# Optimization experiments

Measured on AMD Instinct MI355X. Metric: run time of the kernel, lower is better.

The kernel has to match this reference:

```python
import jax, jax.numpy as jnp
import numpy as np

B, T, C = 2, 2048, 2048
H = 16
D = C // H  # head_dim = 128


def rotate_half(x):
    x1, x2 = jnp.split(x, 2, axis=-1)
    return jnp.concatenate([-x2, x1], axis=-1)


def apply_rotary(q, k, cos, sin):
    # q,k: (B,H,T,D); cos,sin: (T,D/2)
    cos2 = jnp.concatenate([cos, cos], axis=-1)[None, None]  # (1,1,T,D)
    sin2 = jnp.concatenate([sin, sin], axis=-1)[None, None]
    return q * cos2 + rotate_half(q) * sin2, k * cos2 + rotate_half(k) * sin2


def setup_inputs() -> dict:
    key = jax.random.key(0)
    k1, k2, k3, k4 = jax.random.split(key, 4)
    x = jax.random.normal(k1, (B, T, C), dtype=jnp.float32)
    w_qkv = jax.random.normal(k2, (C, 3 * C), dtype=jnp.float32) * (C ** -0.5)
    w_out = jax.random.normal(k3, (C, C), dtype=jnp.float32) * (C ** -0.5)
    pos = jnp.arange(T, dtype=jnp.float32)[:, None]
    inv_freq = 1.0 / (10000.0 ** (jnp.arange(0, D, 2, dtype=jnp.float32) / D))  # (D/2,)
    ang = pos * inv_freq[None, :]  # (T, D/2)
    return {"x": x, "w_qkv": w_qkv, "w_out": w_out,
            "cos": jnp.cos(ang), "sin": jnp.sin(ang)}


def reference(x, w_qkv, w_out, cos, sin):
    b, t, c = x.shape
    qkv = x @ w_qkv  # (B,T,3C)
    qkv = qkv.reshape(b, t, 3, H, D)
    q, k, v = qkv[:, :, 0], qkv[:, :, 1], qkv[:, :, 2]  # (B,T,H,D)
    q = q.transpose(0, 2, 1, 3)  # (B,H,T,D)
    k = k.transpose(0, 2, 1, 3)
    v = v.transpose(0, 2, 1, 3)
    q, k = apply_rotary(q, k, cos, sin)
    scale = 1.0 / jnp.sqrt(jnp.asarray(D, dtype=x.dtype))
    scores = jnp.einsum('bhqd,bhkd->bhqk', q, k) * scale  # (B,H,T,T)
    causal = jnp.tril(jnp.ones((t, t), dtype=bool))
    scores = jnp.where(causal[None, None], scores, jnp.asarray(-jnp.inf, dtype=scores.dtype))
    attn = jax.nn.softmax(scores, axis=-1)
    out = jnp.einsum('bhqk,bhkd->bhqd', attn, v)  # (B,H,T,D)
    out = out.transpose(0, 2, 1, 3).reshape(b, t, c)
    return out @ w_out
```

## Files before the change

### kernel.cpp

```cpp
#include <hip/hip_runtime.h>


typedef __attribute__((ext_vector_type(8))) short short8;
typedef __attribute__((ext_vector_type(4))) float floatx4;
typedef __attribute__((ext_vector_type(4))) unsigned int uint4v;

#define MFMA16(a, b, c) __builtin_amdgcn_mfma_f32_16x16x32_bf16(a, b, c, 0, 0, 0)

__device__ inline unsigned short f2bf(float f) {
    union { float f; unsigned int i; } v; v.f = f;
    unsigned int r = v.i + 0x7fff + ((v.i >> 16) & 1);
    return (unsigned short)(r >> 16);
}

__device__ inline void gl2lds16(const unsigned short* g, unsigned short* l) {
    __builtin_amdgcn_global_load_lds(
        (const __attribute__((address_space(1))) unsigned int*)g,
        (__attribute__((address_space(3))) unsigned int*)l, 16, 0, 0);
}

__device__ __forceinline__ void bar_lds_only() {
    asm volatile("s_waitcnt lgkmcnt(0)" ::: "memory");
    __builtin_amdgcn_sched_barrier(0);
    __builtin_amdgcn_s_barrier();
    __builtin_amdgcn_sched_barrier(0);
}

__global__ __launch_bounds__(256) void cvt_k(const float* __restrict__ in,
                                             unsigned short* __restrict__ out, int n) {
    int i = (blockIdx.x * 256 + threadIdx.x) * 8;
    if (i + 7 < n) {
        float4 v0 = *(const float4*)(&in[i]);
        float4 v1 = *(const float4*)(&in[i + 4]);
        ushort4 o0, o1;
        o0.x = f2bf(v0.x); o0.y = f2bf(v0.y); o0.z = f2bf(v0.z); o0.w = f2bf(v0.w);
        o1.x = f2bf(v1.x); o1.y = f2bf(v1.y); o1.z = f2bf(v1.z); o1.w = f2bf(v1.w);
        *(ushort4*)(&out[i])     = o0;
        *(ushort4*)(&out[i + 4]) = o1;
    } else {
        for (int j = i; j < n; j++) out[j] = f2bf(in[j]);
    }
}

__global__ __launch_bounds__(256) void transpose_f2b_k(const float* __restrict__ in,
                                                       unsigned short* __restrict__ out,
                                                       int R, int Cc) {
    __shared__ unsigned short tile[32][33];
    int ct = blockIdx.x * 32;
    int rt = blockIdx.y * 32;
    int tx = threadIdx.x & 31;
    int ty = threadIdx.x >> 5;
#pragma unroll
    for (int i = 0; i < 32; i += 8)
        tile[ty + i][tx] = f2bf(in[(size_t)(rt + ty + i) * Cc + ct + tx]);
    __syncthreads();
#pragma unroll
    for (int i = 0; i < 32; i += 8)
        out[(size_t)(ct + ty + i) * R + rt + tx] = tile[tx][ty + i];
}

__global__ __launch_bounds__(256) void transpose_v_k(const unsigned short* __restrict__ qkv,
                                                     unsigned short* __restrict__ VT) {
    __shared__ unsigned short tile[32][33];
    int t0 = blockIdx.x * 32;
    int d0 = blockIdx.y * 32;
    int bh = blockIdx.z;
    int b = bh >> 4, h = bh & 15;
    int tx = threadIdx.x & 31;
    int ty = threadIdx.x >> 5;
#pragma unroll
    for (int i = 0; i < 32; i += 8)
        tile[ty + i][tx] =
            qkv[((size_t)(b * 2048 + t0 + ty + i) * 3 + 2) * 2048 + h * 128 + d0 + tx];
    __syncthreads();
#pragma unroll
    for (int i = 0; i < 32; i += 8)
        VT[((size_t)bh * 128 + d0 + ty + i) * 2048 + t0 + tx] = tile[tx][ty + i];
}

__global__ __launch_bounds__(256) void rotary_k(unsigned short* qkv,
                                                const float* __restrict__ cosT,
                                                const float* __restrict__ sinT) {
    int idx = blockIdx.x * 256 + threadIdx.x;
    int d    = idx & 63;
    int h    = (idx >> 6) & 15;
    int part = (idx >> 10) & 1;
    int t    = (idx >> 11) & 2047;
    int b    = idx >> 22;
    size_t base = ((size_t)(b * 2048 + t) * 3 + part) * 2048 + h * 128;
    float c = cosT[t * 64 + d];
    float s = sinT[t * 64 + d];
    union { unsigned int i; float f; } u1, u2;
    u1.i = ((unsigned int)qkv[base + d]) << 16;
    u2.i = ((unsigned int)qkv[base + d + 64]) << 16;
    float x1 = u1.f, x2 = u2.f;
    qkv[base + d]      = f2bf(x1 * c - x2 * s);
    qkv[base + d + 64] = f2bf(x2 * c + x1 * s);
}

template <bool OUTF32>
__global__ __launch_bounds__(256) void gemm_bt(const unsigned short* __restrict__ A, long lda,
                                               const unsigned short* __restrict__ Bt,
                                               void* __restrict__ Co, long ldc,
                                               int M, int N, int K) {
    __shared__ unsigned short a_lds[2][128 * 32];
    __shared__ unsigned short b_lds[2][128 * 32];
    int m0 = blockIdx.y * 128, n0 = blockIdx.x * 128;
    int tid = threadIdx.x;
    int lane = tid & 63, w = tid >> 6;
    int wm = (w >> 1) * 64, wn = (w & 1) * 64;
    int lr = lane & 15, quad = lane >> 4, lk = quad * 8;

    floatx4 acc[4][4];
    floatx4 zero4 = {0.f, 0.f, 0.f, 0.f};
#pragma unroll
    for (int i = 0; i < 4; i++)
#pragma unroll
        for (int j = 0; j < 4; j++) acc[i][j] = zero4;

    auto stage = [&](int k0, int buf) {
#pragma unroll
        for (int i = 0; i < 2; i++) {
            int c = w * 128 + i * 64 + lane;
            int row = c >> 2, seg = (c & 3) * 8;
            gl2lds16(&A[(size_t)(m0 + row) * lda + k0 + seg], &a_lds[buf][c * 8]);
            gl2lds16(&Bt[(size_t)(n0 + row) * K + k0 + seg], &b_lds[buf][c * 8]);
        }
    };

    int nt = K >> 5;
    stage(0, 0);
    __syncthreads();
    for (int t = 0; t < nt; t++) {
        int buf = t & 1;
        if (t + 1 < nt) stage((t + 1) * 32, buf ^ 1);
        short8 af[4], bfr[4];
#pragma unroll
        for (int i = 0; i < 4; i++)
            af[i] = *(const short8*)(&a_lds[buf][(wm + i * 16 + lr) * 32 + lk]);
#pragma unroll
        for (int j = 0; j < 4; j++)
            bfr[j] = *(const short8*)(&b_lds[buf][(wn + j * 16 + lr) * 32 + lk]);
#pragma unroll
        for (int i = 0; i < 4; i++)
#pragma unroll
            for (int j = 0; j < 4; j++)
                acc[i][j] = MFMA16(af[i], bfr[j], acc[i][j]);
        __syncthreads();
    }
#pragma unroll
    for (int i = 0; i < 4; i++)
#pragma unroll
        for (int j = 0; j < 4; j++)
#pragma unroll
            for (int r = 0; r < 4; r++) {
                int row = m0 + wm + i * 16 + quad * 4 + r;
                int col = n0 + wn + j * 16 + lr;
                if (OUTF32)
                    ((float*)Co)[(size_t)row * ldc + col] = acc[i][j][r];
                else
                    ((unsigned short*)Co)[(size_t)row * ldc + col] = f2bf(acc[i][j][r]);
            }
}

__device__ __forceinline__ void attn_core(const short8 (&qf)[4], floatx4 (&o_acc)[8],
                                          floatx4& o_l,
                                          float (&m_i)[4],
                                          const unsigned short* kb_lds,
                                          const unsigned short* vb_lds,
                                          unsigned short* p_w,
                                          int qrow0, int tk0, int lr, int quad, int lk) {
    floatx4 zero4 = {0.f, 0.f, 0.f, 0.f};
    const float scale = 0.08838834764831845f;

    floatx4 s[4];
#pragma unroll
    for (int n = 0; n < 4; n++) {
        s[n] = zero4;
#pragma unroll
        for (int c = 0; c < 4; c++) {
            short8 kb = *(const short8*)(
                &kb_lds[(n * 16 + lr) * 128 + (((c * 4 + quad) ^ lr) * 8)]);
            s[n] = MFMA16(qf[c], kb, s[n]);
        }
    }

    float rmax[4];
#pragma unroll
    for (int r = 0; r < 4; r++) {
        int tqr = qrow0 + quad * 4 + r;
        float mx = -1e30f;
#pragma unroll
        for (int n = 0; n < 4; n++) {
            int tk = tk0 + n * 16 + lr;
            float sv = s[n][r] * scale;
            sv = (tk > tqr) ? -1e30f : sv;
            s[n][r] = sv;
            mx = fmaxf(mx, sv);
        }
        rmax[r] = mx;
    }
#pragma unroll
    for (int off = 1; off < 16; off <<= 1)
#pragma unroll
        for (int r = 0; r < 4; r++)
            rmax[r] = fmaxf(rmax[r], __shfl_xor(rmax[r], off, 64));

    float alpha[4];
#pragma unroll
    for (int r = 0; r < 4; r++) {
        float mn = fmaxf(m_i[r], rmax[r]);
        alpha[r] = __expf(m_i[r] - mn);
        m_i[r] = mn;
    }
#pragma unroll
    for (int n = 0; n < 4; n++)
#pragma unroll
        for (int r = 0; r < 4; r++) {
            float p = __expf(s[n][r] - m_i[r]);
            p_w[(quad * 4 + r) * 72 + n * 16 + lr] = f2bf(p);
        }

#pragma unroll
    for (int dt = 0; dt < 8; dt++)
#pragma unroll
        for (int r = 0; r < 4; r++) o_acc[dt][r] *= alpha[r];
#pragma unroll
    for (int r = 0; r < 4; r++) o_l[r] *= alpha[r];

    short8 pa[2];
#pragma unroll
    for (int kc = 0; kc < 2; kc++)
        pa[kc] = *(const short8*)(&p_w[lr * 72 + kc * 32 + lk]);
#pragma unroll
    for (int dt = 0; dt < 8; dt++) {
#pragma unroll
        for (int kc = 0; kc < 2; kc++) {
            short8 vb = *(const short8*)(
                &vb_lds[(dt * 16 + lr) * 64 + (((kc * 4 + quad) ^ (lr & 7)) * 8)]);
            o_acc[dt] = MFMA16(pa[kc], vb, o_acc[dt]);
        }
    }
#pragma unroll
    for (int kc = 0; kc < 2; kc++) {
        short8 vb1 = *(const short8*)(&vb_lds[128 * 64 + (kc * 4 + quad) * 8]);
        o_l = MFMA16(pa[kc], vb1, o_l);
    }
}

__global__ __launch_bounds__(512, 4) void attn_fast(unsigned short* qkv,
                                                    const unsigned short* __restrict__ VT) {
    const int T = 2048, Cc = 2048, Dd = 128;
    int xx = blockIdx.x;
    int qt = (xx & 1) ? (xx >> 1) : (15 - (xx >> 1));
    int bh = blockIdx.y;
    int b = bh >> 4, h = bh & 15;
    int tid = threadIdx.x, lane = tid & 63, w = tid >> 6;
    int lr = lane & 15, quad = lane >> 4, lk = quad * 8;
    int t0 = qt * 128;

    __shared__ __align__(16) unsigned short k_lds[64 * 128];
    __shared__ __align__(16) unsigned short v_lds[129 * 64];
    __shared__ __align__(16) unsigned short p_lds[8][16][72];

    if (tid < 64) v_lds[128 * 64 + tid] = 0x3F80;

    short8 qf[4];
    {
        size_t qrow = (size_t)(b * T + t0 + w * 16 + lr) * 3 * Cc + h * Dd;
#pragma unroll
        for (int c = 0; c < 4; c++)
            qf[c] = *(const short8*)(&qkv[qrow + c * 32 + lk]);
    }

    floatx4 o_acc[8];
    floatx4 zero4 = {0.f, 0.f, 0.f, 0.f};
#pragma unroll
    for (int i = 0; i < 8; i++) o_acc[i] = zero4;
    floatx4 o_l = zero4;
    float m_i[4];
#pragma unroll
    for (int r = 0; r < 4; r++) m_i[r] = -1e30f;

    int krow[2], kslot[2], vrow[2], vslot[2];
#pragma unroll
    for (int i = 0; i < 2; i++) {
        int c = i * 512 + tid;
        krow[i] = c >> 4; kslot[i] = c & 15;
        vrow[i] = c >> 3; vslot[i] = c & 7;
    }
    uint4v kA[2], vA[2];
    auto gload = [&](int kt) {
        int tk0 = kt * 64;
#pragma unroll
        for (int i = 0; i < 2; i++) {
            kA[i] = *(const uint4v*)(
                &qkv[((size_t)(b * T + tk0 + krow[i]) * 3 + 1) * Cc + h * Dd + kslot[i] * 8]);
            vA[i] = *(const uint4v*)(
                &VT[((size_t)bh * Dd + vrow[i]) * T + tk0 + vslot[i] * 8]);
        }
    };
    auto lwrite = [&]() {
#pragma unroll
        for (int i = 0; i < 2; i++) {
            *(uint4v*)(&k_lds[krow[i] * 128 + ((kslot[i] ^ (krow[i] & 15)) * 8)]) = kA[i];
            *(uint4v*)(&v_lds[vrow[i] * 64 + ((vslot[i] ^ (vrow[i] & 7)) * 8)]) = vA[i];
        }
    };

    int nkt = 2 * qt + 2;
    gload(0);

    for (int kt = 0; kt < nkt; kt++) {
        lwrite();
        bar_lds_only();
        if (kt + 1 < nkt) gload(kt + 1);
        int tk0 = kt * 64;
        if (tk0 <= t0 + w * 16 + 15)
            attn_core(qf, o_acc, o_l, m_i, k_lds, v_lds, &p_lds[w][0][0],
                      t0 + w * 16, tk0, lr, quad, lk);
        bar_lds_only();
    }

#pragma unroll
    for (int dt = 0; dt < 8; dt++)
#pragma unroll
        for (int r = 0; r < 4; r++) {
            int row = t0 + w * 16 + quad * 4 + r;
            int col = dt * 16 + lr;
            qkv[(size_t)(b * T + row) * 3 * Cc + h * Dd + col] = f2bf(o_acc[dt][r] * (1.0f / o_l[r]));
        }
}

extern "C" void kernel_launch(void* const* d_in, const int* in_sizes, int n_in,
                              void* d_out, int out_size, void* d_ws, size_t ws_size,
                              hipStream_t stream) {
    const float* x    = (const float*)d_in[0];
    const float* wqkv = (const float*)d_in[1];
    const float* wout = (const float*)d_in[2];
    const float* cosT = (const float*)d_in[3];
    const float* sinT = (const float*)d_in[4];
    float* out = (float*)d_out;

    unsigned short* qkv = (unsigned short*)d_ws;
    const size_t QKV = 25165824, XBF = 8388608;
    unsigned short* xbf = qkv + QKV;
    unsigned short* wTq = xbf + XBF;
    unsigned short* VT  = xbf;
    unsigned short* wTo = wTq;

    cvt_k<<<4096, 256, 0, stream>>>(x, xbf, 8388608);
    transpose_f2b_k<<<dim3(192, 64), 256, 0, stream>>>(wqkv, wTq, 2048, 6144);
    gemm_bt<false><<<dim3(48, 32), 256, 0, stream>>>(xbf, 2048, wTq, qkv, 6144,
                                                     4096, 6144, 2048);
    rotary_k<<<32768, 256, 0, stream>>>(qkv, cosT, sinT);
    transpose_f2b_k<<<dim3(64, 64), 256, 0, stream>>>(wout, wTo, 2048, 2048);
    transpose_v_k<<<dim3(64, 4, 32), 256, 0, stream>>>(qkv, VT);
    attn_fast<<<dim3(16, 32), 512, 0, stream>>>(qkv, VT);
    gemm_bt<true><<<dim3(16, 32), 256, 0, stream>>>(qkv, 6144, wTo, out, 2048,
                                                    4096, 2048, 2048);
}
```

Measured before the change: 454.6 us.

## Process two 16-row query tiles per wave in attention to reuse K/V fragments

The attention block shrinks from 8 waves to 4, and each wave now handles 32 query rows as two 16-row sub-tiles that share every K and V fragment read from LDS. This roughly halves LDS fragment reads per MFMA and doubles the global-to-LDS load work per thread. The cost is higher register pressure from doubled accumulators, fewer waves per block, and coarser causal skipping, since a wave now runs whenever any of its 32 rows needs the tile.

```diff
diff --git a/kernel.cpp b/kernel.cpp
--- a/kernel.cpp
+++ b/kernel.cpp
@@ -163,92 +163,108 @@
             }
 }
 
-__device__ __forceinline__ void attn_core(const short8 (&qf)[4], floatx4 (&o_acc)[8],
-                                          floatx4& o_l,
-                                          float (&m_i)[4],
-                                          const unsigned short* kb_lds,
-                                          const unsigned short* vb_lds,
-                                          unsigned short* p_w,
-                                          int qrow0, int tk0, int lr, int quad, int lk) {
+__device__ __forceinline__ void attn_core_pair(
+        const short8 (&qfA)[4], const short8 (&qfB)[4],
+        floatx4 (&oA)[8], floatx4 (&oB)[8], floatx4& olA, floatx4& olB,
+        float (&mA)[4], float (&mB)[4],
+        const unsigned short* kb_lds, const unsigned short* vb_lds,
+        unsigned short* p_w,
+        int qrow0, int tk0, int lr, int quad, int lk) {
     floatx4 zero4 = {0.f, 0.f, 0.f, 0.f};
     const float scale = 0.08838834764831845f;
 
-    floatx4 s[4];
+    floatx4 sA[4], sB[4];
 #pragma unroll
     for (int n = 0; n < 4; n++) {
-        s[n] = zero4;
+        sA[n] = zero4; sB[n] = zero4;
 #pragma unroll
         for (int c = 0; c < 4; c++) {
             short8 kb = *(const short8*)(
                 &kb_lds[(n * 16 + lr) * 128 + (((c * 4 + quad) ^ lr) * 8)]);
-            s[n] = MFMA16(qf[c], kb, s[n]);
-        }
-    }
-
-    float rmax[4];
+            sA[n] = MFMA16(qfA[c], kb, sA[n]);
+            sB[n] = MFMA16(qfB[c], kb, sB[n]);
+        }
+    }
+
+    float rmaxA[4], rmaxB[4];
 #pragma unroll
     for (int r = 0; r < 4; r++) {
-        int tqr = qrow0 + quad * 4 + r;
-        float mx = -1e30f;
+        int tqA = qrow0 + quad * 4 + r;
+        int tqB = tqA + 16;
+        float mxA = -1e30f, mxB = -1e30f;
 #pragma unroll
         for (int n = 0; n < 4; n++) {
             int tk = tk0 + n * 16 + lr;
-            float sv = s[n][r] * scale;
-            sv = (tk > tqr) ? -1e30f : sv;
-            s[n][r] = sv;
-            mx = fmaxf(mx, sv);
-        }
-        rmax[r] = mx;
+            float svA = sA[n][r] * scale;
+            float svB = sB[n][r] * scale;
+            svA = (tk > tqA) ? -1e30f : svA;
+            svB = (tk > tqB) ? -1e30f : svB;
+            sA[n][r] = svA; sB[n][r] = svB;
+            mxA = fmaxf(mxA, svA); mxB = fmaxf(mxB, svB);
+        }
+        rmaxA[r] = mxA; rmaxB[r] = mxB;
     }
 #pragma unroll
     for (int off = 1; off < 16; off <<= 1)
 #pragma unroll
-        for (int r = 0; r < 4; r++)
-            rmax[r] = fmaxf(rmax[r], __shfl_xor(rmax[r], off, 64));
-
-    float alpha[4];
+        for (int r = 0; r < 4; r++) {
+            rmaxA[r] = fmaxf(rmaxA[r], __shfl_xor(rmaxA[r], off, 64));
+            rmaxB[r] = fmaxf(rmaxB[r], __shfl_xor(rmaxB[r], off, 64));
+        }
+
+    float alphaA[4], alphaB[4];
 #pragma unroll
     for (int r = 0; r < 4; r++) {
-        float mn = fmaxf(m_i[r], rmax[r]);
-        alpha[r] = __expf(m_i[r] - mn);
-        m_i[r] = mn;
+        float mnA = fmaxf(mA[r], rmaxA[r]);
+        float mnB = fmaxf(mB[r], rmaxB[r]);
+        alphaA[r] = __expf(mA[r] - mnA); mA[r] = mnA;
+        alphaB[r] = __expf(mB[r] - mnB); mB[r] = mnB;
     }
 #pragma unroll
     for (int n = 0; n < 4; n++)
 #pragma unroll
         for (int r = 0; r < 4; r++) {
-            float p = __expf(s[n][r] - m_i[r]);
-            p_w[(quad * 4 + r) * 72 + n * 16 + lr] = f2bf(p);
+            float pA = __expf(sA[n][r] - mA[r]);
+            float pB = __expf(sB[n][r] - mB[r]);
+            p_w[(quad * 4 + r) * 72 + n * 16 + lr] = f2bf(pA);
+            p_w[(16 + quad * 4 + r) * 72 + n * 16 + lr] = f2bf(pB);
         }
 
 #pragma unroll
     for (int dt = 0; dt < 8; dt++)
 #pragma unroll
-        for (int r = 0; r < 4; r++) o_acc[dt][r] *= alpha[r];
-#pragma unroll
-    for (int r = 0; r < 4; r++) o_l[r] *= alpha[r];
-
-    short8 pa[2];
-#pragma unroll
-    for (int kc = 0; kc < 2; kc++)
-        pa[kc] = *(const short8*)(&p_w[lr * 72 + kc * 32 + lk]);
+        for (int r = 0; r < 4; r++) {
+            oA[dt][r] *= alphaA[r];
+            oB[dt][r] *= alphaB[r];
+        }
+#pragma unroll
+    for (int r = 0; r < 4; r++) { olA[r] *= alphaA[r]; olB[r] *= alphaB[r]; }
+
+    short8 paA[2], paB[2];
+#pragma unroll
+    for (int kc = 0; kc < 2; kc++) {
+        paA[kc] = *(const short8*)(&p_w[lr * 72 + kc * 32 + lk]);
+        paB[kc] = *(const short8*)(&p_w[(16 + lr) * 72 + kc * 32 + lk]);
+    }
 #pragma unroll
     for (int dt = 0; dt < 8; dt++) {
 #pragma unroll
         for (int kc = 0; kc < 2; kc++) {
             short8 vb = *(const short8*)(
                 &vb_lds[(dt * 16 + lr) * 64 + (((kc * 4 + quad) ^ (lr & 7)) * 8)]);
-            o_acc[dt] = MFMA16(pa[kc], vb, o_acc[dt]);
+            oA[dt] = MFMA16(paA[kc], vb, oA[dt]);
+            oB[dt] = MFMA16(paB[kc], vb, oB[dt]);
         }
     }
 #pragma unroll
     for (int kc = 0; kc < 2; kc++) {
         short8 vb1 = *(const short8*)(&vb_lds[128 * 64 + (kc * 4 + quad) * 8]);
-        o_l = MFMA16(pa[kc], vb1, o_l);
-    }
-}
-
-__global__ __launch_bounds__(512, 4) void attn_fast(unsigned short* qkv,
+        olA = MFMA16(paA[kc], vb1, olA);
+        olB = MFMA16(paB[kc], vb1, olB);
+    }
+}
+
+__global__ __launch_bounds__(256, 2) void attn_fast(unsigned short* qkv,
                                                     const unsigned short* __restrict__ VT) {
     const int T = 2048, Cc = 2048, Dd = 128;
     int xx = blockIdx.x;
@@ -258,42 +274,46 @@
     int tid = threadIdx.x, lane = tid & 63, w = tid >> 6;
     int lr = lane & 15, quad = lane >> 4, lk = quad * 8;
     int t0 = qt * 128;
+    int wrow = t0 + w * 32;
 
     __shared__ __align__(16) unsigned short k_lds[64 * 128];
     __shared__ __align__(16) unsigned short v_lds[129 * 64];
-    __shared__ __align__(16) unsigned short p_lds[8][16][72];
+    __shared__ __align__(16) unsigned short p_lds[4][32][72];
 
     if (tid < 64) v_lds[128 * 64 + tid] = 0x3F80;
 
-    short8 qf[4];
+    short8 qfA[4], qfB[4];
     {
-        size_t qrow = (size_t)(b * T + t0 + w * 16 + lr) * 3 * Cc + h * Dd;
-#pragma unroll
-        for (int c = 0; c < 4; c++)
-            qf[c] = *(const short8*)(&qkv[qrow + c * 32 + lk]);
-    }
-
-    floatx4 o_acc[8];
+        size_t qrA = (size_t)(b * T + wrow + lr) * 3 * Cc + h * Dd;
+        size_t qrB = (size_t)(b * T + wrow + 16 + lr) * 3 * Cc + h * Dd;
+#pragma unroll
+        for (int c = 0; c < 4; c++) {
+            qfA[c] = *(const short8*)(&qkv[qrA + c * 32 + lk]);
+            qfB[c] = *(const short8*)(&qkv[qrB + c * 32 + lk]);
+        }
+    }
+
+    floatx4 oA[8], oB[8];
     floatx4 zero4 = {0.f, 0.f, 0.f, 0.f};
 #pragma unroll
-    for (int i = 0; i < 8; i++) o_acc[i] = zero4;
-    floatx4 o_l = zero4;
-    float m_i[4];
-#pragma unroll
-    for (int r = 0; r < 4; r++) m_i[r] = -1e30f;
-
-    int krow[2], kslot[2], vrow[2], vslot[2];
-#pragma unroll
-    for (int i = 0; i < 2; i++) {
-        int c = i * 512 + tid;
+    for (int i = 0; i < 8; i++) { oA[i] = zero4; oB[i] = zero4; }
+    floatx4 olA = zero4, olB = zero4;
+    float mA[4], mB[4];
+#pragma unroll
+    for (int r = 0; r < 4; r++) { mA[r] = -1e30f; mB[r] = -1e30f; }
+
+    int krow[4], kslot[4], vrow[4], vslot[4];
+#pragma unroll
+    for (int i = 0; i < 4; i++) {
+        int c = i * 256 + tid;
         krow[i] = c >> 4; kslot[i] = c & 15;
         vrow[i] = c >> 3; vslot[i] = c & 7;
     }
-    uint4v kA[2], vA[2];
+    uint4v kA[4], vA[4];
     auto gload = [&](int kt) {
         int tk0 = kt * 64;
 #pragma unroll
-        for (int i = 0; i < 2; i++) {
+        for (int i = 0; i < 4; i++) {
             kA[i] = *(const uint4v*)(
                 &qkv[((size_t)(b * T + tk0 + krow[i]) * 3 + 1) * Cc + h * Dd + kslot[i] * 8]);
             vA[i] = *(const uint4v*)(
@@ -302,7 +322,7 @@
     };
     auto lwrite = [&]() {
 #pragma unroll
-        for (int i = 0; i < 2; i++) {
+        for (int i = 0; i < 4; i++) {
             *(uint4v*)(&k_lds[krow[i] * 128 + ((kslot[i] ^ (krow[i] & 15)) * 8)]) = kA[i];
             *(uint4v*)(&v_lds[vrow[i] * 64 + ((vslot[i] ^ (vrow[i] & 7)) * 8)]) = vA[i];
         }
@@ -316,9 +336,9 @@
         bar_lds_only();
         if (kt + 1 < nkt) gload(kt + 1);
         int tk0 = kt * 64;
-        if (tk0 <= t0 + w * 16 + 15)
-            attn_core(qf, o_acc, o_l, m_i, k_lds, v_lds, &p_lds[w][0][0],
-                      t0 + w * 16, tk0, lr, quad, lk);
+        if (tk0 <= wrow + 31)
+            attn_core_pair(qfA, qfB, oA, oB, olA, olB, mA, mB,
+                           k_lds, v_lds, &p_lds[w][0][0], wrow, tk0, lr, quad, lk);
         bar_lds_only();
     }
 
@@ -326,9 +346,13 @@
     for (int dt = 0; dt < 8; dt++)
 #pragma unroll
         for (int r = 0; r < 4; r++) {
-            int row = t0 + w * 16 + quad * 4 + r;
             int col = dt * 16 + lr;
-            qkv[(size_t)(b * T + row) * 3 * Cc + h * Dd + col] = f2bf(o_acc[dt][r] * (1.0f / o_l[r]));
+            int rowA = wrow + quad * 4 + r;
+            int rowB = rowA + 16;
+            qkv[(size_t)(b * T + rowA) * 3 * Cc + h * Dd + col] =
+                f2bf(oA[dt][r] * (1.0f / olA[r]));
+            qkv[(size_t)(b * T + rowB) * 3 * Cc + h * Dd + col] =
+                f2bf(oB[dt][r] * (1.0f / olB[r]));
         }
 }
 
@@ -356,7 +380,7 @@
     rotary_k<<<32768, 256, 0, stream>>>(qkv, cosT, sinT);
     transpose_f2b_k<<<dim3(64, 64), 256, 0, stream>>>(wout, wTo, 2048, 2048);
     transpose_v_k<<<dim3(64, 4, 32), 256, 0, stream>>>(qkv, VT);
-    attn_fast<<<dim3(16, 32), 512, 0, stream>>>(qkv, VT);
+    attn_fast<<<dim3(16, 32), 256, 0, stream>>>(qkv, VT);
     gemm_bt<true><<<dim3(16, 32), 256, 0, stream>>>(qkv, 6144, wTo, out, 2048,
                                                     4096, 2048, 2048);
 }
```

Result: no change. 448.8 us (-1.3%).
